# Performance work log

Hardware: AMD Instinct MI355X
Metric: run time of the kernel (lower is better)

## Reference

```python
import jax, jax.numpy as jnp
import numpy as np

N_NODES = 50000
N_EDGES = 800000
D_IN = 96
D_OUT = 96
K_ORDER = 3


def setup_inputs() -> dict:
    key = jax.random.key(0)
    k1, k2, k3, k4, k5 = jax.random.split(key, 5)
    rows = jax.random.randint(k1, (N_EDGES,), 0, N_NODES, dtype=jnp.int64 if jax.config.jax_enable_x64 else jnp.int32)
    cols = jax.random.randint(k2, (N_EDGES,), 0, N_NODES, dtype=jnp.int64 if jax.config.jax_enable_x64 else jnp.int32)
    vals = jax.random.uniform(k3, (N_EDGES,), dtype=jnp.float32) * (1.0 / 16.0)  # ~sym-normalized weights
    H = jax.random.normal(k4, (N_NODES, D_IN), dtype=jnp.float32)
    W = jax.random.normal(k5, (D_IN, D_OUT), dtype=jnp.float32) * (1.0 / np.sqrt(D_IN))
    bias = jnp.zeros((D_OUT,), dtype=jnp.float32)
    return {"rows": rows, "cols": cols, "vals": vals, "H": H, "W": W, "bias": bias}


def reference(rows, cols, vals, H, W, bias):
    n = H.shape[0]

    def spmm(X):  # L @ X via gather-multiply-scatter over COO edges
        return jax.ops.segment_sum(vals[:, None] * X[cols], rows, num_segments=n)

    def ln_mm(X):  # (2L - I) @ X
        return 2.0 * spmm(X) - X

    # k = 0 term: T_0 = H
    H_out = H @ W
    # k = 1 term: T_1 = (2L - I) H  (differentiable, as in torch code)
    T_prev = H
    T_curr = ln_mm(H)
    H_out = H_out + T_curr @ W
    # k >= 2: recurrence computed under no_grad in the original -> stop_gradient
    for _ in range(2, K_ORDER + 1):
        T_next = jax.lax.stop_gradient(2.0 * ln_mm(T_curr) - T_prev)
        H_out = H_out + T_next @ W
        T_prev, T_curr = T_curr, T_next
    return H_out + bias
```

## Files before the change

### kernel.cpp

```cpp
#include <hip/hip_runtime.h>
#include <hip/hip_fp16.h>

#define NN 50000
#define NE 800000
#define D  96
#define NB_SCAN 196
#define N4 (NN * D / 4)
#define CB4 ((N4 + 255) / 256)
#define WFRAG_BLKS 5

typedef unsigned int   uint32;
typedef unsigned short uint16;
typedef short  v8s __attribute__((ext_vector_type(8)));
typedef float  v4f __attribute__((ext_vector_type(4)));
typedef unsigned int v2u __attribute__((ext_vector_type(2)));

__device__ inline uint16 f32_to_bf16(float f) {
    uint32 u = __float_as_uint(f);
    u += 0x7FFF + ((u >> 16) & 1);
    return (uint16)(u >> 16);
}

__device__ inline void u2f(v2u u, float& a, float& b, float& c, float& d) {
    a = __uint_as_float(u.x << 16);
    b = __uint_as_float(u.x & 0xFFFF0000u);
    c = __uint_as_float(u.y << 16);
    d = __uint_as_float(u.y & 0xFFFF0000u);
}

__device__ inline float f16_val(uint32 e) {
    __half_raw h; h.x = (uint16)(e >> 16);
    return __half2float(__half(h));
}

__global__ void prep(const float4* __restrict__ H, ushort4* __restrict__ Hb,
                     const float* __restrict__ W, uint16* __restrict__ Wfrag,
                     int* __restrict__ counts) {
    int b = blockIdx.x;
    int t = threadIdx.x;
    if (b < CB4) {
        int i = b * 256 + t;
        if (i < N4) {
            float4 v = H[i];
            ushort4 o;
            o.x = f32_to_bf16(v.x); o.y = f32_to_bf16(v.y);
            o.z = f32_to_bf16(v.z); o.w = f32_to_bf16(v.w);
            Hb[i] = o;
        }
    } else if (b < CB4 + NB_SCAN) {
        int i = (b - CB4) * 256 + t;
        if (i < NN) counts[i] = 0;
    } else {
        int idx = (b - CB4 - NB_SCAN) * 256 + t;
        if (idx < 18 * 64) {
            int bt = idx >> 6, lane = idx & 63;
            int nt = bt / 3, kc = bt % 3;
            int col = nt * 16 + (lane & 15);
            int kbase = kc * 32 + (lane >> 4) * 8;
            uint16 tmp[8];
            #pragma unroll
            for (int j = 0; j < 8; ++j) tmp[j] = f32_to_bf16(W[(kbase + j) * D + col]);
            uint32* dst = (uint32*)(Wfrag + ((size_t)bt * 64 + lane) * 8);
            const uint32* src = (const uint32*)tmp;
            #pragma unroll
            for (int j = 0; j < 4; ++j) dst[j] = src[j];
        }
    }
}

__global__ void hist_slots(const int* __restrict__ rows, int* __restrict__ counts,
                           int* __restrict__ slot) {
    int e = blockIdx.x * blockDim.x + threadIdx.x;
    if (e < NE) slot[e] = atomicAdd(&counts[rows[e]], 1);
}

__global__ void scan_p1(const int* __restrict__ counts, int* __restrict__ partials) {
    __shared__ int red[256];
    int t = threadIdx.x;
    int i = blockIdx.x * 256 + t;
    red[t] = (i < NN) ? counts[i] : 0;
    __syncthreads();
    for (int off = 128; off > 0; off >>= 1) {
        if (t < off) red[t] += red[t + off];
        __syncthreads();
    }
    if (t == 0) partials[blockIdx.x] = red[0];
}

__global__ void scan_p23(const int* __restrict__ counts, const int* __restrict__ partials,
                         int* __restrict__ row_ptr) {
    __shared__ int pp[256];
    __shared__ int sh[256];
    int t = threadIdx.x;
    pp[t] = (t < NB_SCAN) ? partials[t] : 0;
    __syncthreads();
    for (int off = 1; off < 256; off <<= 1) {
        int u = (t >= off) ? pp[t - off] : 0;
        __syncthreads();
        pp[t] += u;
        __syncthreads();
    }
    int blk_off = (blockIdx.x == 0) ? 0 : pp[blockIdx.x - 1];
    int i = blockIdx.x * 256 + t;
    int v = (i < NN) ? counts[i] : 0;
    sh[t] = v;
    __syncthreads();
    for (int off = 1; off < 256; off <<= 1) {
        int u = (t >= off) ? sh[t - off] : 0;
        __syncthreads();
        sh[t] += u;
        __syncthreads();
    }
    int excl = sh[t] - v + blk_off;
    if (i < NN) row_ptr[i] = excl;
    if (i == NN - 1) row_ptr[NN] = excl + v;
}

__global__ void fill_edges(const int* __restrict__ rows, const int* __restrict__ cols,
                           const float* __restrict__ vals, const int* __restrict__ row_ptr,
                           const int* __restrict__ slot, uint32* __restrict__ edges) {
    int e = blockIdx.x * blockDim.x + threadIdx.x;
    if (e < NE) {
        int p = row_ptr[rows[e]] + slot[e];
        __half_raw hr = __half_raw(__float2half(vals[e]));
        edges[p] = (uint32)(cols[e] & 0xFFFF) | ((uint32)hr.x << 16);
    }
}

__global__ void spmm(const int* __restrict__ row_ptr, const uint32* __restrict__ edges,
                     const uint16* __restrict__ Xb, const uint16* __restrict__ A,
                     const uint16* __restrict__ B, uint16* __restrict__ Yb,
                     float scale, float ca, float cb) {
    int tid  = threadIdx.x;
    int lane = tid & 31;
    int g    = tid >> 5;
    int r = blockIdx.x * 8 + g;
    if (r >= NN) return;
    if (lane >= 24) return;

    const v2u* xbase = (const v2u*)Xb;

    v2u av = __builtin_nontemporal_load((const v2u*)(A + (size_t)r * D) + lane);
    v2u bv = __builtin_nontemporal_load((const v2u*)(B + (size_t)r * D) + lane);
    float a0,a1,a2,a3,b0,b1,b2,b3;
    u2f(av, a0,a1,a2,a3);
    u2f(bv, b0,b1,b2,b3);
    float ax = ca*a0 + cb*b0;
    float ay = ca*a1 + cb*b1;
    float az = ca*a2 + cb*b2;
    float aw = ca*a3 + cb*b3;

    int s = row_ptr[r];
    int e = row_ptr[r + 1];
    int i = s;
    for (; i + 7 < e; i += 8) {
        uint32 ee[8];
        #pragma unroll
        for (int j = 0; j < 8; ++j) ee[j] = edges[i + j];
        v2u xx[8];
        #pragma unroll
        for (int j = 0; j < 8; ++j)
            xx[j] = xbase[(size_t)(ee[j] & 0xFFFF) * 24 + lane];
        #pragma unroll
        for (int j = 0; j < 8; ++j) {
            float v = scale * f16_val(ee[j]);
            float x0,x1,x2,x3;
            u2f(xx[j], x0,x1,x2,x3);
            ax += v*x0; ay += v*x1; az += v*x2; aw += v*x3;
        }
    }
    for (; i + 3 < e; i += 4) {
        uint32 ee[4];
        #pragma unroll
        for (int j = 0; j < 4; ++j) ee[j] = edges[i + j];
        v2u xx[4];
        #pragma unroll
        for (int j = 0; j < 4; ++j)
            xx[j] = xbase[(size_t)(ee[j] & 0xFFFF) * 24 + lane];
        #pragma unroll
        for (int j = 0; j < 4; ++j) {
            float v = scale * f16_val(ee[j]);
            float x0,x1,x2,x3;
            u2f(xx[j], x0,x1,x2,x3);
            ax += v*x0; ay += v*x1; az += v*x2; aw += v*x3;
        }
    }
    for (; i < e; ++i) {
        uint32 e0 = edges[i];
        float v = scale * f16_val(e0);
        v2u x = xbase[(size_t)(e0 & 0xFFFF) * 24 + lane];
        float x0,x1,x2,x3;
        u2f(x, x0,x1,x2,x3);
        ax += v*x0; ay += v*x1; az += v*x2; aw += v*x3;
    }

    v2u o;
    o.x = (uint32)f32_to_bf16(ax) | ((uint32)f32_to_bf16(ay) << 16);
    o.y = (uint32)f32_to_bf16(az) | ((uint32)f32_to_bf16(aw) << 16);
    __builtin_nontemporal_store(o, (v2u*)(Yb + (size_t)r * D) + lane);
}

__global__ void mfma_gemm(const uint16* __restrict__ Sb, const uint16* __restrict__ Wfrag,
                          const float* __restrict__ bias, float* __restrict__ out) {
    int tid   = threadIdx.x;
    int lane  = tid & 63;
    int wv    = blockIdx.x * (blockDim.x >> 6) + (tid >> 6);
    int nwv   = gridDim.x * (blockDim.x >> 6);
    int col   = lane & 15;
    int quad  = lane >> 4;

    v8s wf[6][3];
    #pragma unroll
    for (int nt = 0; nt < 6; ++nt)
        #pragma unroll
        for (int kc = 0; kc < 3; ++kc)
            wf[nt][kc] = ((const v8s*)Wfrag)[(nt * 3 + kc) * 64 + lane];

    float bi[6];
    #pragma unroll
    for (int nt = 0; nt < 6; ++nt) bi[nt] = bias[nt * 16 + col];

    for (int s = wv; s < NN / 16; s += nwv) {
        int r0 = s * 16;
        const uint16* arow = Sb + (size_t)(r0 + col) * D + quad * 8;
        v8s a0 = *((const v8s*)(arow));
        v8s a1 = *((const v8s*)(arow + 32));
        v8s a2 = *((const v8s*)(arow + 64));
        v4f acc[6];
        #pragma unroll
        for (int nt = 0; nt < 6; ++nt) {
            v4f c = {0.f, 0.f, 0.f, 0.f};
            c = __builtin_amdgcn_mfma_f32_16x16x32_bf16(a0, wf[nt][0], c, 0, 0, 0);
            c = __builtin_amdgcn_mfma_f32_16x16x32_bf16(a1, wf[nt][1], c, 0, 0, 0);
            c = __builtin_amdgcn_mfma_f32_16x16x32_bf16(a2, wf[nt][2], c, 0, 0, 0);
            acc[nt] = c;
        }
        #pragma unroll
        for (int nt = 0; nt < 6; ++nt) {
            float* o = out + (size_t)(r0 + quad * 4) * D + nt * 16 + col;
            o[0 * D] = acc[nt][0] + bi[nt];
            o[1 * D] = acc[nt][1] + bi[nt];
            o[2 * D] = acc[nt][2] + bi[nt];
            o[3 * D] = acc[nt][3] + bi[nt];
        }
    }
}

extern "C" void kernel_launch(void* const* d_in, const int* in_sizes, int n_in,
                              void* d_out, int out_size, void* d_ws, size_t ws_size,
                              hipStream_t stream) {
    const int*   rows = (const int*)d_in[0];
    const int*   cols = (const int*)d_in[1];
    const float* vals = (const float*)d_in[2];
    const float* H    = (const float*)d_in[3];
    const float* W    = (const float*)d_in[4];
    const float* bias = (const float*)d_in[5];
    float* out = (float*)d_out;

    char* ws = (char*)d_ws;
    uint16* Hb       = (uint16*)ws;  ws += (size_t)NN * D * 2;
    uint16* T1b      = (uint16*)ws;  ws += (size_t)NN * D * 2;
    uint16* T2b      = (uint16*)ws;  ws += (size_t)NN * D * 2;
    uint32* edges    = (uint32*)ws;  ws += (size_t)NE * 4;
    uint16* Wfrag    = (uint16*)ws;  ws += (size_t)18 * 64 * 8 * 2;
    int*    counts   = (int*)ws;     ws += (size_t)NN * 4;
    int*    row_ptr  = (int*)ws;     ws += (size_t)(NN + 1) * 4;
    int*    partials = (int*)ws;     ws += 256 * 4;
    int*    slot     = (int*)T2b;
    uint16* Sb       = T1b;

    const int eb = (NE + 255) / 256;

    prep<<<CB4 + NB_SCAN + WFRAG_BLKS, 256, 0, stream>>>(
        (const float4*)H, (ushort4*)Hb, W, Wfrag, counts);
    hist_slots<<<eb, 256, 0, stream>>>(rows, counts, slot);
    scan_p1<<<NB_SCAN, 256, 0, stream>>>(counts, partials);
    scan_p23<<<NB_SCAN, 256, 0, stream>>>(counts, partials, row_ptr);
    fill_edges<<<eb, 256, 0, stream>>>(rows, cols, vals, row_ptr, slot, edges);

    const int sb = (NN + 7) / 8;

    spmm<<<sb, 256, 0, stream>>>(row_ptr, edges, Hb, Hb, Hb, T1b, 2.0f, -1.0f, 0.0f);
    spmm<<<sb, 256, 0, stream>>>(row_ptr, edges, T1b, T1b, Hb, T2b, 4.0f, -2.0f, -1.0f);
    spmm<<<sb, 256, 0, stream>>>(row_ptr, edges, T2b, Hb, T2b, Sb, 4.0f, 1.0f, -1.0f);
    mfma_gemm<<<391, 256, 0, stream>>>(Sb, Wfrag, bias, out);
}
```

Baseline: 237.2 us.

## Rewrite Chebyshev sum as monomial powers of L combined in GEMM

The Chebyshev recurrence is expanded algebraically, so the summed polynomial becomes 12·LH − 40·L²H + 32·L³H. Each SpMM now computes a plain L·X product, with no per-row reads of two previous terms and no scaling. The final GEMM kernel reads the three power buffers and forms the weighted combination in registers before the MFMA. This removes six bf16 row-stream reads from the SpMM passes and adds two extra reads in the GEMM, plus one more workspace buffer. The monomial basis with large cancelling coefficients over bf16-stored intermediates may lose accuracy.

```diff
diff --git a/kernel.cpp b/kernel.cpp
--- a/kernel.cpp
+++ b/kernel.cpp
@@ -14,6 +14,7 @@
 typedef short  v8s __attribute__((ext_vector_type(8)));
 typedef float  v4f __attribute__((ext_vector_type(4)));
 typedef unsigned int v2u __attribute__((ext_vector_type(2)));
+typedef unsigned int v4u __attribute__((ext_vector_type(4)));
 
 __device__ inline uint16 f32_to_bf16(float f) {
     uint32 u = __float_as_uint(f);
@@ -31,6 +32,15 @@
 __device__ inline float f16_val(uint32 e) {
     __half_raw h; h.x = (uint16)(e >> 16);
     return __half2float(__half(h));
+}
+
+__device__ inline uint32 comb2(uint32 u1, uint32 u2, uint32 u3) {
+    float a1 = __uint_as_float(u1 << 16), b1 = __uint_as_float(u1 & 0xFFFF0000u);
+    float a2 = __uint_as_float(u2 << 16), b2 = __uint_as_float(u2 & 0xFFFF0000u);
+    float a3 = __uint_as_float(u3 << 16), b3 = __uint_as_float(u3 & 0xFFFF0000u);
+    float sa = 12.f * a1 - 40.f * a2 + 32.f * a3;
+    float sb = 12.f * b1 - 40.f * b2 + 32.f * b3;
+    return (uint32)f32_to_bf16(sa) | ((uint32)f32_to_bf16(sb) << 16);
 }
 
 __global__ void prep(const float4* __restrict__ H, ushort4* __restrict__ Hb,
@@ -128,9 +138,7 @@
 }
 
 __global__ void spmm(const int* __restrict__ row_ptr, const uint32* __restrict__ edges,
-                     const uint16* __restrict__ Xb, const uint16* __restrict__ A,
-                     const uint16* __restrict__ B, uint16* __restrict__ Yb,
-                     float scale, float ca, float cb) {
+                     const uint16* __restrict__ Xb, uint16* __restrict__ Yb) {
     int tid  = threadIdx.x;
     int lane = tid & 31;
     int g    = tid >> 5;
@@ -140,15 +148,7 @@
 
     const v2u* xbase = (const v2u*)Xb;
 
-    v2u av = __builtin_nontemporal_load((const v2u*)(A + (size_t)r * D) + lane);
-    v2u bv = __builtin_nontemporal_load((const v2u*)(B + (size_t)r * D) + lane);
-    float a0,a1,a2,a3,b0,b1,b2,b3;
-    u2f(av, a0,a1,a2,a3);
-    u2f(bv, b0,b1,b2,b3);
-    float ax = ca*a0 + cb*b0;
-    float ay = ca*a1 + cb*b1;
-    float az = ca*a2 + cb*b2;
-    float aw = ca*a3 + cb*b3;
+    float ax = 0.f, ay = 0.f, az = 0.f, aw = 0.f;
 
     int s = row_ptr[r];
     int e = row_ptr[r + 1];
@@ -163,7 +163,7 @@
             xx[j] = xbase[(size_t)(ee[j] & 0xFFFF) * 24 + lane];
         #pragma unroll
         for (int j = 0; j < 8; ++j) {
-            float v = scale * f16_val(ee[j]);
+            float v = f16_val(ee[j]);
             float x0,x1,x2,x3;
             u2f(xx[j], x0,x1,x2,x3);
             ax += v*x0; ay += v*x1; az += v*x2; aw += v*x3;
@@ -179,7 +179,7 @@
             xx[j] = xbase[(size_t)(ee[j] & 0xFFFF) * 24 + lane];
         #pragma unroll
         for (int j = 0; j < 4; ++j) {
-            float v = scale * f16_val(ee[j]);
+            float v = f16_val(ee[j]);
             float x0,x1,x2,x3;
             u2f(xx[j], x0,x1,x2,x3);
             ax += v*x0; ay += v*x1; az += v*x2; aw += v*x3;
@@ -187,7 +187,7 @@
     }
     for (; i < e; ++i) {
         uint32 e0 = edges[i];
-        float v = scale * f16_val(e0);
+        float v = f16_val(e0);
         v2u x = xbase[(size_t)(e0 & 0xFFFF) * 24 + lane];
         float x0,x1,x2,x3;
         u2f(x, x0,x1,x2,x3);
@@ -200,7 +200,8 @@
     __builtin_nontemporal_store(o, (v2u*)(Yb + (size_t)r * D) + lane);
 }
 
-__global__ void mfma_gemm(const uint16* __restrict__ Sb, const uint16* __restrict__ Wfrag,
+__global__ void mfma_gemm(const uint16* __restrict__ U1, const uint16* __restrict__ U2,
+                          const uint16* __restrict__ U3, const uint16* __restrict__ Wfrag,
                           const float* __restrict__ bias, float* __restrict__ out) {
     int tid   = threadIdx.x;
     int lane  = tid & 63;
@@ -222,17 +223,25 @@
 
     for (int s = wv; s < NN / 16; s += nwv) {
         int r0 = s * 16;
-        const uint16* arow = Sb + (size_t)(r0 + col) * D + quad * 8;
-        v8s a0 = *((const v8s*)(arow));
-        v8s a1 = *((const v8s*)(arow + 32));
-        v8s a2 = *((const v8s*)(arow + 64));
+        size_t base = (size_t)(r0 + col) * D + quad * 8;
+        v8s a[3];
+        #pragma unroll
+        for (int kc = 0; kc < 3; ++kc) {
+            v4u u1 = *(const v4u*)(U1 + base + kc * 32);
+            v4u u2 = *(const v4u*)(U2 + base + kc * 32);
+            v4u u3 = *(const v4u*)(U3 + base + kc * 32);
+            v4u sres;
+            #pragma unroll
+            for (int j = 0; j < 4; ++j) sres[j] = comb2(u1[j], u2[j], u3[j]);
+            a[kc] = __builtin_bit_cast(v8s, sres);
+        }
         v4f acc[6];
         #pragma unroll
         for (int nt = 0; nt < 6; ++nt) {
             v4f c = {0.f, 0.f, 0.f, 0.f};
-            c = __builtin_amdgcn_mfma_f32_16x16x32_bf16(a0, wf[nt][0], c, 0, 0, 0);
-            c = __builtin_amdgcn_mfma_f32_16x16x32_bf16(a1, wf[nt][1], c, 0, 0, 0);
-            c = __builtin_amdgcn_mfma_f32_16x16x32_bf16(a2, wf[nt][2], c, 0, 0, 0);
+            c = __builtin_amdgcn_mfma_f32_16x16x32_bf16(a[0], wf[nt][0], c, 0, 0, 0);
+            c = __builtin_amdgcn_mfma_f32_16x16x32_bf16(a[1], wf[nt][1], c, 0, 0, 0);
+            c = __builtin_amdgcn_mfma_f32_16x16x32_bf16(a[2], wf[nt][2], c, 0, 0, 0);
             acc[nt] = c;
         }
         #pragma unroll
@@ -259,15 +268,15 @@
 
     char* ws = (char*)d_ws;
     uint16* Hb       = (uint16*)ws;  ws += (size_t)NN * D * 2;
-    uint16* T1b      = (uint16*)ws;  ws += (size_t)NN * D * 2;
-    uint16* T2b      = (uint16*)ws;  ws += (size_t)NN * D * 2;
+    uint16* U1b      = (uint16*)ws;  ws += (size_t)NN * D * 2;
+    uint16* U2b      = (uint16*)ws;  ws += (size_t)NN * D * 2;
+    uint16* U3b      = (uint16*)ws;  ws += (size_t)NN * D * 2;
     uint32* edges    = (uint32*)ws;  ws += (size_t)NE * 4;
     uint16* Wfrag    = (uint16*)ws;  ws += (size_t)18 * 64 * 8 * 2;
     int*    counts   = (int*)ws;     ws += (size_t)NN * 4;
     int*    row_ptr  = (int*)ws;     ws += (size_t)(NN + 1) * 4;
     int*    partials = (int*)ws;     ws += 256 * 4;
-    int*    slot     = (int*)T2b;
-    uint16* Sb       = T1b;
+    int*    slot     = (int*)U2b;
 
     const int eb = (NE + 255) / 256;
 
@@ -280,8 +289,8 @@
 
     const int sb = (NN + 7) / 8;
 
-    spmm<<<sb, 256, 0, stream>>>(row_ptr, edges, Hb, Hb, Hb, T1b, 2.0f, -1.0f, 0.0f);
-    spmm<<<sb, 256, 0, stream>>>(row_ptr, edges, T1b, T1b, Hb, T2b, 4.0f, -2.0f, -1.0f);
-    spmm<<<sb, 256, 0, stream>>>(row_ptr, edges, T2b, Hb, T2b, Sb, 4.0f, 1.0f, -1.0f);
-    mfma_gemm<<<391, 256, 0, stream>>>(Sb, Wfrag, bias, out);
-}
+    spmm<<<sb, 256, 0, stream>>>(row_ptr, edges, Hb,  U1b);
+    spmm<<<sb, 256, 0, stream>>>(row_ptr, edges, U1b, U2b);
+    spmm<<<sb, 256, 0, stream>>>(row_ptr, edges, U2b, U3b);
+    mfma_gemm<<<391, 256, 0, stream>>>(U1b, U2b, U3b, Wfrag, bias, out);
+}
```

Measured after the change: 231.4 us. -2.5%, faster.
